# Optimization experiments

Hardware: AMD Instinct MI355X
Metric: run time of the kernel (lower is better)

The kernel has to match this reference:

```python
import jax, jax.numpy as jnp
import numpy as np

NUM_QUANT_BITS = 8


def setup_inputs() -> dict:
    key = jax.random.key(0)
    x = jax.random.normal(key, (64, 56, 56, 256), dtype=jnp.float32)
    return {"x": x}


def reference(x):
    # Global range (min_val/max_val default to None in the original layer)
    min_val = jnp.min(x)
    max_val = jnp.max(x)
    quantized_range = jnp.asarray(2 ** NUM_QUANT_BITS - 1, dtype=x.dtype)  # 255
    scale = quantized_range / (max_val - min_val)
    xc = jnp.clip(x, min_val, max_val)
    # round-to-nearest-even matches tf.round semantics
    out = jnp.round((xc - min_val) * scale) / scale + min_val
    return out
```

## Files before the change

kernel.cpp:

```cpp
#include <hip/hip_runtime.h>
#include <stdint.h>
#include <math.h>

typedef float vf4 __attribute__((ext_vector_type(4)));

__device__ __forceinline__ uint32_t enc_f32(float f) {
    uint32_t b = __float_as_uint(f);
    return (b & 0x80000000u) ? ~b : (b | 0x80000000u);
}
__device__ __forceinline__ float dec_f32(uint32_t u) {
    uint32_t b = (u & 0x80000000u) ? (u ^ 0x80000000u) : ~u;
    return __uint_as_float(b);
}

__global__ void init_ws_kernel(uint32_t* ws) {
    ws[0] = 0xFFFFFFFFu;
    ws[1] = 0x00000000u;
}

__device__ __forceinline__ void mm4(vf4 v, float& mn, float& mx) {
    mn = fminf(mn, fminf(fminf(v.x, v.y), fminf(v.z, v.w)));
    mx = fmaxf(mx, fmaxf(fmaxf(v.x, v.y), fmaxf(v.z, v.w)));
}

__global__ __launch_bounds__(256) void minmax_kernel(
    const vf4* __restrict__ x4, unsigned n4,
    uint32_t* __restrict__ ws)
{
    float mn0 = INFINITY, mn1 = INFINITY, mn2 = INFINITY, mn3 = INFINITY;
    float mx0 = -INFINITY, mx1 = -INFINITY, mx2 = -INFINITY, mx3 = -INFINITY;

    const unsigned bs = blockDim.x;
    const unsigned stride = gridDim.x * bs * 4u;
    unsigned base = blockIdx.x * bs * 4u + threadIdx.x;

    for (; base + 3u * bs < n4; base += stride) {
        vf4 v0 = x4[base];
        vf4 v1 = x4[base + bs];
        vf4 v2 = x4[base + 2u * bs];
        vf4 v3 = x4[base + 3u * bs];
        mm4(v0, mn0, mx0);
        mm4(v1, mn1, mx1);
        mm4(v2, mn2, mx2);
        mm4(v3, mn3, mx3);
    }
    for (; base < n4; base += bs) {
        mm4(x4[base], mn0, mx0);
    }

    float mn = fminf(fminf(mn0, mn1), fminf(mn2, mn3));
    float mx = fmaxf(fmaxf(mx0, mx1), fmaxf(mx2, mx3));

    #pragma unroll
    for (int off = 32; off > 0; off >>= 1) {
        mn = fminf(mn, __shfl_down(mn, off, 64));
        mx = fmaxf(mx, __shfl_down(mx, off, 64));
    }
    __shared__ float smn[4], smx[4];
    const int wave = threadIdx.x >> 6;
    const int lane = threadIdx.x & 63;
    if (lane == 0) { smn[wave] = mn; smx[wave] = mx; }
    __syncthreads();
    if (threadIdx.x == 0) {
        mn = fminf(fminf(smn[0], smn[1]), fminf(smn[2], smn[3]));
        mx = fmaxf(fmaxf(smx[0], smx[1]), fmaxf(smx[2], smx[3]));
        atomicMin(&ws[0], enc_f32(mn));
        atomicMax(&ws[1], enc_f32(mx));
    }
}

__device__ __forceinline__ vf4 q4(vf4 v, float mn, float scale, float inv_scale) {
    vf4 r;
    r.x = rintf((v.x - mn) * scale) * inv_scale + mn;
    r.y = rintf((v.y - mn) * scale) * inv_scale + mn;
    r.z = rintf((v.z - mn) * scale) * inv_scale + mn;
    r.w = rintf((v.w - mn) * scale) * inv_scale + mn;
    return r;
}

__global__ __launch_bounds__(256) void quant_kernel(
    const vf4* __restrict__ x4, unsigned n4,
    vf4* __restrict__ o4,
    const uint32_t* __restrict__ ws)
{
    const float mn = dec_f32(ws[0]);
    const float mx = dec_f32(ws[1]);
    const float scale = 255.0f / (mx - mn);
    const float inv_scale = 1.0f / scale;

    const unsigned bs = blockDim.x;
    const unsigned stride = gridDim.x * bs * 4u;
    unsigned base = blockIdx.x * bs * 4u + threadIdx.x;

    for (; base + 3u * bs < n4; base += stride) {
        vf4 v0 = x4[base];
        vf4 v1 = x4[base + bs];
        vf4 v2 = x4[base + 2u * bs];
        vf4 v3 = x4[base + 3u * bs];
        __builtin_nontemporal_store(q4(v0, mn, scale, inv_scale), &o4[base]);
        __builtin_nontemporal_store(q4(v1, mn, scale, inv_scale), &o4[base + bs]);
        __builtin_nontemporal_store(q4(v2, mn, scale, inv_scale), &o4[base + 2u * bs]);
        __builtin_nontemporal_store(q4(v3, mn, scale, inv_scale), &o4[base + 3u * bs]);
    }
    for (; base < n4; base += bs) {
        __builtin_nontemporal_store(q4(x4[base], mn, scale, inv_scale), &o4[base]);
    }
}

__global__ void quant_tail_kernel(const float* __restrict__ x, long start, long n,
                                  float* __restrict__ o,
                                  const uint32_t* __restrict__ ws)
{
    const float mn = dec_f32(ws[0]);
    const float mx = dec_f32(ws[1]);
    const float scale = 255.0f / (mx - mn);
    const float inv_scale = 1.0f / scale;
    long i = start + threadIdx.x;
    if (i < n) o[i] = rintf((x[i] - mn) * scale) * inv_scale + mn;
}

__global__ void minmax_tail_kernel(const float* __restrict__ x, long start, long n,
                                   uint32_t* __restrict__ ws)
{
    long i = start + threadIdx.x;
    if (i < n) {
        float v = x[i];
        atomicMin(&ws[0], enc_f32(v));
        atomicMax(&ws[1], enc_f32(v));
    }
}

extern "C" void kernel_launch(void* const* d_in, const int* in_sizes, int n_in,
                              void* d_out, int out_size, void* d_ws, size_t ws_size,
                              hipStream_t stream) {
    const float* x = (const float*)d_in[0];
    float* out = (float*)d_out;
    const long n = (long)in_sizes[0];
    const unsigned n4 = (unsigned)(n / 4);
    uint32_t* ws = (uint32_t*)d_ws;

    init_ws_kernel<<<1, 1, 0, stream>>>(ws);

    const int block = 256;
    const int grid = 2048;

    minmax_kernel<<<grid, block, 0, stream>>>((const vf4*)x, n4, ws);
    if (n % 4) minmax_tail_kernel<<<1, 256, 0, stream>>>(x, (long)n4 * 4, n, ws);

    quant_kernel<<<grid, block, 0, stream>>>((const vf4*)x, n4, (vf4*)out, ws);
    if (n % 4) quant_tail_kernel<<<1, 256, 0, stream>>>(x, (long)n4 * 4, n, out, ws);
}
```

Baseline: 375.0 us.

## Fuse min/max reduction and quantization into one cooperative kernel with grid sync

Replaces the init, minmax and quant kernel sequence with a single cooperative kernel. Each block writes its partial min/max to workspace, a grid-wide sync follows, then every block reduces the partials and quantizes. This removes separate launches and the global atomics, and is sized so re-reading x may hit in cache. It depends on cooperative launch support and enough workspace, and falls back to the old path otherwise. Grid.sync adds a barrier cost, and the grid is capped by occupancy.

```diff
diff --git a/kernel.cpp b/kernel.cpp
--- a/kernel.cpp
+++ b/kernel.cpp
@@ -1,39 +1,45 @@
 #include <hip/hip_runtime.h>
+#include <hip/hip_cooperative_groups.h>
 #include <stdint.h>
 #include <math.h>
 
+namespace cg = cooperative_groups;
+
 typedef float vf4 __attribute__((ext_vector_type(4)));
-
-__device__ __forceinline__ uint32_t enc_f32(float f) {
-    uint32_t b = __float_as_uint(f);
-    return (b & 0x80000000u) ? ~b : (b | 0x80000000u);
-}
-__device__ __forceinline__ float dec_f32(uint32_t u) {
-    uint32_t b = (u & 0x80000000u) ? (u ^ 0x80000000u) : ~u;
-    return __uint_as_float(b);
-}
-
-__global__ void init_ws_kernel(uint32_t* ws) {
-    ws[0] = 0xFFFFFFFFu;
-    ws[1] = 0x00000000u;
-}
 
 __device__ __forceinline__ void mm4(vf4 v, float& mn, float& mx) {
     mn = fminf(mn, fminf(fminf(v.x, v.y), fminf(v.z, v.w)));
     mx = fmaxf(mx, fmaxf(fmaxf(v.x, v.y), fmaxf(v.z, v.w)));
 }
 
-__global__ __launch_bounds__(256) void minmax_kernel(
-    const vf4* __restrict__ x4, unsigned n4,
-    uint32_t* __restrict__ ws)
-{
+__device__ __forceinline__ vf4 q4(vf4 v, float mn, float scale, float inv_scale) {
+    vf4 r;
+    r.x = rintf((v.x - mn) * scale) * inv_scale + mn;
+    r.y = rintf((v.y - mn) * scale) * inv_scale + mn;
+    r.z = rintf((v.z - mn) * scale) * inv_scale + mn;
+    r.w = rintf((v.w - mn) * scale) * inv_scale + mn;
+    return r;
+}
+
+__global__ __launch_bounds__(256, 4) void fused_fakequant(
+    const float* __restrict__ x, long n,
+    float* __restrict__ o,
+    float* __restrict__ ws)
+{
+    const vf4* __restrict__ x4 = (const vf4*)x;
+    vf4* __restrict__ o4 = (vf4*)o;
+    const unsigned n4 = (unsigned)(n >> 2);
+
+    cg::grid_group grid = cg::this_grid();
+    const unsigned bs = blockDim.x;
+    const unsigned nb = gridDim.x;
+    const unsigned tid = threadIdx.x;
+
     float mn0 = INFINITY, mn1 = INFINITY, mn2 = INFINITY, mn3 = INFINITY;
     float mx0 = -INFINITY, mx1 = -INFINITY, mx2 = -INFINITY, mx3 = -INFINITY;
 
-    const unsigned bs = blockDim.x;
-    const unsigned stride = gridDim.x * bs * 4u;
-    unsigned base = blockIdx.x * bs * 4u + threadIdx.x;
-
+    const unsigned stride = nb * bs * 4u;
+    unsigned base = blockIdx.x * bs * 4u + tid;
     for (; base + 3u * bs < n4; base += stride) {
         vf4 v0 = x4[base];
         vf4 v1 = x4[base + bs];
@@ -44,13 +50,106 @@
         mm4(v2, mn2, mx2);
         mm4(v3, mn3, mx3);
     }
-    for (; base < n4; base += bs) {
-        mm4(x4[base], mn0, mx0);
+    for (; base < n4; base += bs) mm4(x4[base], mn0, mx0);
+    for (long i = (long)n4 * 4 + (long)blockIdx.x * bs + tid; i < n;
+         i += (long)nb * bs) {
+        float v = x[i];
+        mn0 = fminf(mn0, v); mx0 = fmaxf(mx0, v);
     }
 
     float mn = fminf(fminf(mn0, mn1), fminf(mn2, mn3));
     float mx = fmaxf(fmaxf(mx0, mx1), fmaxf(mx2, mx3));
-
+    #pragma unroll
+    for (int off = 32; off > 0; off >>= 1) {
+        mn = fminf(mn, __shfl_down(mn, off, 64));
+        mx = fmaxf(mx, __shfl_down(mx, off, 64));
+    }
+    __shared__ float smn[4], smx[4];
+    const int wave = tid >> 6;
+    const int lane = tid & 63;
+    if (lane == 0) { smn[wave] = mn; smx[wave] = mx; }
+    __syncthreads();
+    if (tid == 0) {
+        ws[blockIdx.x]      = fminf(fminf(smn[0], smn[1]), fminf(smn[2], smn[3]));
+        ws[nb + blockIdx.x] = fmaxf(fmaxf(smx[0], smx[1]), fmaxf(smx[2], smx[3]));
+    }
+
+    grid.sync();
+
+    float gmn = INFINITY, gmx = -INFINITY;
+    for (unsigned i = tid; i < nb; i += bs) {
+        gmn = fminf(gmn, ws[i]);
+        gmx = fmaxf(gmx, ws[nb + i]);
+    }
+    #pragma unroll
+    for (int off = 32; off > 0; off >>= 1) {
+        gmn = fminf(gmn, __shfl_down(gmn, off, 64));
+        gmx = fmaxf(gmx, __shfl_down(gmx, off, 64));
+    }
+    if (lane == 0) { smn[wave] = gmn; smx[wave] = gmx; }
+    __syncthreads();
+    const float fmn = fminf(fminf(smn[0], smn[1]), fminf(smn[2], smn[3]));
+    const float fmx = fmaxf(fmaxf(smx[0], smx[1]), fmaxf(smx[2], smx[3]));
+    const float scale = 255.0f / (fmx - fmn);
+    const float inv_scale = 1.0f / scale;
+
+    base = blockIdx.x * bs * 4u + tid;
+    for (; base + 3u * bs < n4; base += stride) {
+        vf4 v0 = x4[base];
+        vf4 v1 = x4[base + bs];
+        vf4 v2 = x4[base + 2u * bs];
+        vf4 v3 = x4[base + 3u * bs];
+        __builtin_nontemporal_store(q4(v0, fmn, scale, inv_scale), &o4[base]);
+        __builtin_nontemporal_store(q4(v1, fmn, scale, inv_scale), &o4[base + bs]);
+        __builtin_nontemporal_store(q4(v2, fmn, scale, inv_scale), &o4[base + 2u * bs]);
+        __builtin_nontemporal_store(q4(v3, fmn, scale, inv_scale), &o4[base + 3u * bs]);
+    }
+    for (; base < n4; base += bs)
+        __builtin_nontemporal_store(q4(x4[base], fmn, scale, inv_scale), &o4[base]);
+    for (long i = (long)n4 * 4 + (long)blockIdx.x * bs + tid; i < n;
+         i += (long)nb * bs)
+        o[i] = rintf((x[i] - fmn) * scale) * inv_scale + fmn;
+}
+
+__device__ __forceinline__ uint32_t enc_f32(float f) {
+    uint32_t b = __float_as_uint(f);
+    return (b & 0x80000000u) ? ~b : (b | 0x80000000u);
+}
+__device__ __forceinline__ float dec_f32(uint32_t u) {
+    uint32_t b = (u & 0x80000000u) ? (u ^ 0x80000000u) : ~u;
+    return __uint_as_float(b);
+}
+
+__global__ void init_ws_kernel(uint32_t* ws) {
+    ws[0] = 0xFFFFFFFFu;
+    ws[1] = 0x00000000u;
+}
+
+__global__ __launch_bounds__(256) void minmax_kernel(
+    const vf4* __restrict__ x4, unsigned n4,
+    uint32_t* __restrict__ ws)
+{
+    float mn0 = INFINITY, mn1 = INFINITY, mn2 = INFINITY, mn3 = INFINITY;
+    float mx0 = -INFINITY, mx1 = -INFINITY, mx2 = -INFINITY, mx3 = -INFINITY;
+
+    const unsigned bs = blockDim.x;
+    const unsigned stride = gridDim.x * bs * 4u;
+    unsigned base = blockIdx.x * bs * 4u + threadIdx.x;
+
+    for (; base + 3u * bs < n4; base += stride) {
+        vf4 v0 = x4[base];
+        vf4 v1 = x4[base + bs];
+        vf4 v2 = x4[base + 2u * bs];
+        vf4 v3 = x4[base + 3u * bs];
+        mm4(v0, mn0, mx0);
+        mm4(v1, mn1, mx1);
+        mm4(v2, mn2, mx2);
+        mm4(v3, mn3, mx3);
+    }
+    for (; base < n4; base += bs) mm4(x4[base], mn0, mx0);
+
+    float mn = fminf(fminf(mn0, mn1), fminf(mn2, mn3));
+    float mx = fmaxf(fmaxf(mx0, mx1), fmaxf(mx2, mx3));
     #pragma unroll
     for (int off = 32; off > 0; off >>= 1) {
         mn = fminf(mn, __shfl_down(mn, off, 64));
@@ -69,15 +168,6 @@
     }
 }
 
-__device__ __forceinline__ vf4 q4(vf4 v, float mn, float scale, float inv_scale) {
-    vf4 r;
-    r.x = rintf((v.x - mn) * scale) * inv_scale + mn;
-    r.y = rintf((v.y - mn) * scale) * inv_scale + mn;
-    r.z = rintf((v.z - mn) * scale) * inv_scale + mn;
-    r.w = rintf((v.w - mn) * scale) * inv_scale + mn;
-    return r;
-}
-
 __global__ __launch_bounds__(256) void quant_kernel(
     const vf4* __restrict__ x4, unsigned n4,
     vf4* __restrict__ o4,
@@ -102,9 +192,8 @@
         __builtin_nontemporal_store(q4(v2, mn, scale, inv_scale), &o4[base + 2u * bs]);
         __builtin_nontemporal_store(q4(v3, mn, scale, inv_scale), &o4[base + 3u * bs]);
     }
-    for (; base < n4; base += bs) {
+    for (; base < n4; base += bs)
         __builtin_nontemporal_store(q4(x4[base], mn, scale, inv_scale), &o4[base]);
-    }
 }
 
 __global__ void quant_tail_kernel(const float* __restrict__ x, long start, long n,
@@ -137,16 +226,41 @@
     float* out = (float*)d_out;
     const long n = (long)in_sizes[0];
     const unsigned n4 = (unsigned)(n / 4);
+
+    static int coop_grid = -2;
+    if (coop_grid == -2) {
+        coop_grid = -1;
+        hipDeviceProp_t props;
+        int dev = 0;
+        if (hipGetDevice(&dev) == hipSuccess &&
+            hipGetDeviceProperties(&props, dev) == hipSuccess &&
+            props.cooperativeLaunch) {
+            int maxb = 0;
+            if (hipOccupancyMaxActiveBlocksPerMultiprocessor(
+                    &maxb, (const void*)fused_fakequant, 256, 0) == hipSuccess &&
+                maxb > 0) {
+                long g = (long)maxb * props.multiProcessorCount;
+                if (g > 2048) g = 2048;
+                coop_grid = (int)g;
+            }
+        }
+    }
+
+    if (coop_grid > 0 && ws_size >= (size_t)coop_grid * 2u * sizeof(float)) {
+        float* wsf = (float*)d_ws;
+        long nn = n;
+        void* args[] = { (void*)&x, (void*)&nn, (void*)&out, (void*)&wsf };
+        hipLaunchCooperativeKernel((void*)fused_fakequant, dim3(coop_grid),
+                                   dim3(256), args, 0, stream);
+        return;
+    }
+
     uint32_t* ws = (uint32_t*)d_ws;
-
     init_ws_kernel<<<1, 1, 0, stream>>>(ws);
-
     const int block = 256;
     const int grid = 2048;
-
     minmax_kernel<<<grid, block, 0, stream>>>((const vf4*)x, n4, ws);
     if (n % 4) minmax_tail_kernel<<<1, 256, 0, stream>>>(x, (long)n4 * 4, n, ws);
-
     quant_kernel<<<grid, block, 0, stream>>>((const vf4*)x, n4, (vf4*)out, ws);
     if (n % 4) quant_tail_kernel<<<1, 256, 0, stream>>>(x, (long)n4 * 4, n, out, ws);
 }
```

After: 466.7 us. 24.5% more time.
